# Kernel optimization log

Measured on AMD Instinct MI355X. Metric: run time of the kernel, lower is better.

## Reference

```python
import jax, jax.numpy as jnp
import numpy as np
import math


def _forward(x, f0, theta, sigma, theta0, fbs, mix, w1, b1, w2, b2, conv_w):
    B, I, H, W = x.shape          # config requires B == I == H (== W here)
    S, O, _ = f0.shape            # config requires O == 1
    # ---- log-Gabor filter bank, fully vectorized over (scale, out, in) ----
    yy = jnp.linspace(-1.0, 1.0, H)[:, None]   # meshgrid 'ij': y along rows
    xx = jnp.linspace(-1.0, 1.0, W)[None, :]
    r = jnp.sqrt(xx ** 2 + yy ** 2 + 1e-6)     # [H,W]
    phi = jnp.arctan2(yy, xx)                  # [H,W]
    lr = jnp.log(r)
    log_gabor = jnp.exp(-(lr - jnp.log(f0)[..., None, None]) ** 2
                        / (2.0 * jnp.log(sigma)[..., None, None] ** 2))
    angular = jnp.exp(-(phi - theta[..., None, None]) ** 2
                      / (2.0 * theta0[..., None, None] ** 2))
    filters = log_gabor * angular              # [S,O,I,H,W]
    # ---- FFT (torch fftshift default shifts ALL dims; jnp matches) ----
    xs = jnp.fft.fftshift(jnp.fft.fft2(x))     # [B,I,H,W] complex64
    # ---- frequency attention (two 1x1 convs + softmax over scales) ----
    h1 = jax.nn.relu(jnp.einsum('bchw,oc->bohw', jnp.abs(xs), w1)
                     + b1[None, :, None, None])
    aw = jax.nn.softmax(jnp.einsum('bchw,sc->bshw', h1, w2)
                        + b2[None, :, None, None], axis=1)   # [B,S,H,W]
    # ---- attention-weighted combine. Faithful to torch broadcasting with
    # O==1 and B==I: attended[0,b,i,h,w] = sum_s xs[b,i]*F[s,0,i]*aw[i,s] ----
    attended = jnp.einsum('bihw,sihw,ishw->bihw', xs, filters[:, 0], aw)[None]
    # ---- dynamic frequency band mask (torch slices dims 2,3 = (Cin,H)) ----
    s_idx = jnp.floor((fbs[0, :, 0] + 1.0) / 2.0 * H).astype(jnp.int32)  # [I]
    e_idx = jnp.floor((fbs[0, :, 1] + 1.0) / 2.0 * H).astype(jnp.int32)
    arI = jnp.arange(I)
    arH = jnp.arange(H)
    mk = (arI[None, :] >= s_idx[:, None]) & (arI[None, :] < e_idx[:, None])  # [J,I]
    mh = (arH[None, :] >= s_idx[:, None]) & (arH[None, :] < e_idx[:, None])  # [J,H]
    mask = (mk[:, :, None] & mh[:, None, :]).astype(x.dtype)                 # [J,I,H]
    attended = attended * mask[None, :, :, :, None]
    # ---- back to spatial domain ----
    x_filtered = jnp.fft.ifft2(jnp.fft.ifftshift(attended)).real  # [1,B,I,H,W]
    # ---- spatial 3x3 conv path ----
    x_spatial = jax.lax.conv_general_dilated(
        x, conv_w, window_strides=(1, 1), padding=((1, 1), (1, 1)),
        dimension_numbers=('NCHW', 'OIHW', 'NCHW'))               # [B,1,H,W]
    return mix * x_filtered + (1.0 - mix) * x_spatial[None]


def setup_inputs() -> dict:
    key = jax.random.key(0)
    ks = jax.random.split(key, 10)
    B = I = H = W = 64
    O, S, HID = 1, 3, 64
    PI = math.pi
    x = jax.random.normal(ks[0], (B, I, H, W), dtype=jnp.float32)
    f0 = jnp.ones((S, O, I), jnp.float32)
    theta0 = jnp.ones((S, O, I), jnp.float32)
    sigma = jax.random.uniform(ks[1], (S, O, I), jnp.float32) * PI
    theta = jax.random.uniform(ks[2], (S, O, I), jnp.float32) * PI
    fbs = jax.random.uniform(ks[3], (O, I, 2), jnp.float32)
    mix = jax.random.uniform(ks[4], (1,), jnp.float32)
    w1 = jax.random.normal(ks[5], (HID, I), jnp.float32) * 0.05
    b1 = jnp.zeros((HID,), jnp.float32)
    w2 = jax.random.normal(ks[6], (S, HID), jnp.float32) * 0.05
    b2 = jnp.zeros((S,), jnp.float32)
    conv_w = jax.random.normal(ks[7], (O, I, 3, 3), jnp.float32) / math.sqrt(I * 9)
    return {'x': x, 'f0': f0, 'theta': theta, 'sigma': sigma, 'theta0': theta0,
            'fbs': fbs, 'mix': mix, 'w1': w1, 'b1': b1, 'w2': w2, 'b2': b2,
            'conv_w': conv_w}


def reference(x, f0, theta, sigma, theta0, fbs, mix, w1, b1, w2, b2, conv_w):
    return _forward(x, f0, theta, sigma, theta0, fbs, mix, w1, b1, w2, b2, conv_w)
```

## Files before the change

### kernel.cpp

```cpp
#include <hip/hip_runtime.h>

#define PI_D 3.14159265358979323846

namespace {
constexpr float CT[33] = {
  1.0000000000f,  0.9951847267f,  0.9807852804f,  0.9569403357f,
  0.9238795325f,  0.8819212643f,  0.8314696123f,  0.7730104534f,
  0.7071067812f,  0.6343932842f,  0.5555702330f,  0.4713967368f,
  0.3826834324f,  0.2902846773f,  0.1950903220f,  0.0980171403f,
  0.0f,          -0.0980171403f, -0.1950903220f, -0.2902846773f,
 -0.3826834324f, -0.4713967368f, -0.5555702330f, -0.6343932842f,
 -0.7071067812f, -0.7730104534f, -0.8314696123f, -0.8819212643f,
 -0.9238795325f, -0.9569403357f, -0.9807852804f, -0.9951847267f,
 -1.0f};
constexpr float STb[33] = {
  0.0f,           0.0980171403f,  0.1950903220f,  0.2902846773f,
  0.3826834324f,  0.4713967368f,  0.5555702330f,  0.6343932842f,
  0.7071067812f,  0.7730104534f,  0.8314696123f,  0.8819212643f,
  0.9238795325f,  0.9569403357f,  0.9807852804f,  0.9951847267f,
  1.0f,           0.9951847267f,  0.9807852804f,  0.9569403357f,
  0.9238795325f,  0.8819212643f,  0.8314696123f,  0.7730104534f,
  0.7071067812f,  0.6343932842f,  0.5555702330f,  0.4713967368f,
  0.3826834324f,  0.2902846773f,  0.1950903220f,  0.0980171403f,
  0.0f};
}

__device__ __forceinline__ void bitrev64(float v[64]) {
#pragma unroll
  for (int i = 0; i < 64; ++i) {
    const int j = (int)(__brev((unsigned)i) >> 26);
    if (j > i) { const float tv = v[i]; v[i] = v[j]; v[j] = tv; }
  }
}

template <bool INV, bool REAL>
__device__ __forceinline__ void fft64_stages(float re[64], float im[64]) {
#pragma unroll
  for (int s = 0; s < 6; ++s) {
    const int half = 1 << s;
    const int m = half << 1;
    const int tstep = 32 >> s;
#pragma unroll
    for (int k = 0; k < 64; k += m) {
#pragma unroll
      for (int j = 0; j < half; ++j) {
        const int ti = j * tstep;
        const int a = k + j, b = k + j + half;
        if (REAL && j == 0) {
          const float tr = re[b];
          re[b] = re[a] - tr;
          re[a] = re[a] + tr;
        } else if (REAL && ti == 16) {
          const float t0 = re[b];
          re[b] = re[a];
          im[b] = t0;
          im[a] = -t0;
        } else {
          float tr, tii;
          if (ti == 0) {
            tr = re[b]; tii = im[b];
          } else if (ti == 16) {
            if (INV) { tr = -im[b]; tii = re[b]; }
            else     { tr =  im[b]; tii = -re[b]; }
          } else {
            const float wr = CT[ti];
            const float wi = INV ? STb[ti] : -STb[ti];
            tr  = re[b] * wr - im[b] * wi;
            tii = re[b] * wi + im[b] * wr;
          }
          re[b] = re[a] - tr;  im[b] = im[a] - tii;
          re[a] = re[a] + tr;  im[a] = im[a] + tii;
        }
      }
    }
  }
}

template <bool INV>
__device__ __forceinline__ void fft64_regs(float re[64], float im[64]) {
  bitrev64(re);
  bitrev64(im);
  fft64_stages<INV, false>(re, im);
}

__device__ __forceinline__ void fft64_fwd_real(float re[64], float im[64]) {
  bitrev64(re);
  fft64_stages<false, true>(re, im);
}

__device__ __forceinline__ void band_from_fbs(const float* __restrict__ fbs,
                                              int c, int& s0, int& e0) {
  s0 = (int)floorf((fbs[2 * c]     + 1.0f) * 0.5f * 64.0f);
  e0 = (int)floorf((fbs[2 * c + 1] + 1.0f) * 0.5f * 64.0f);
}

__global__ __launch_bounds__(64) void k_fft_fwd(const float* __restrict__ x,
                                                float* __restrict__ Mag,
                                                float* __restrict__ Fc,
                                                const float* __restrict__ fbs,
                                                const float* __restrict__ w1,
                                                float* __restrict__ w1T) {
  __shared__ float buf[64][65];
  const int t = threadIdx.x;
  const int img = blockIdx.x;
  if (img == 0) {
    for (int k = 0; k < 64; ++k) w1T[t * 64 + k] = w1[k * 64 + t];
  }
  const float* xp = x + ((size_t)img << 12);
  const float4* xr4 = reinterpret_cast<const float4*>(xp + (t << 6));
  float re[64], im[64];
#pragma unroll
  for (int q = 0; q < 16; ++q) {
    const float4 v = xr4[q];
    re[4 * q]     = v.x; re[4 * q + 1] = v.y;
    re[4 * q + 2] = v.z; re[4 * q + 3] = v.w;
  }
#pragma unroll
  for (int j = 0; j < 64; ++j) im[j] = 0.0f;
  fft64_fwd_real(re, im);
#pragma unroll
  for (int j = 0; j < 64; ++j) buf[t][j] = re[j];
  __syncthreads();
#pragma unroll
  for (int j = 0; j < 64; ++j) re[j] = buf[j][t];
  __syncthreads();
#pragma unroll
  for (int j = 0; j < 64; ++j) buf[t][j] = im[j];
  __syncthreads();
#pragma unroll
  for (int j = 0; j < 64; ++j) im[j] = buf[j][t];
  fft64_regs<false>(re, im);
  float* Mg = Mag + ((size_t)img << 12);
  Mg[t] = sqrtf(re[0] * re[0] + im[0] * im[0]);
#pragma unroll
  for (int j = 33; j < 64; ++j)
    Mg[j * 64 + t] = sqrtf(re[j] * re[j] + im[j] * im[j]);
  const int b = img >> 6, i = img & 63;
  const int b_s = (b + 32) & 63, i_s = (i + 32) & 63;
  int s0, e0;
  band_from_fbs(fbs, b_s, s0, e0);
  if ((i_s >= s0) && (i_s < e0)) {
    float* Fre = Fc + ((size_t)((b << 5) + i) << 13);
    float* Fim = Fre + 4096;
#pragma unroll
    for (int j = 0; j < 64; ++j) {
      Fre[j * 64 + t] = re[j];
      Fim[j * 64 + t] = im[j];
    }
  }
}

__global__ __launch_bounds__(256, 4) void k_attn_conv(
    const float* __restrict__ Mag, const float* __restrict__ w1T,
    const float* __restrict__ b1, const float* __restrict__ w2,
    const float* __restrict__ b2, const float* __restrict__ f0,
    const float* __restrict__ theta, const float* __restrict__ sigma,
    const float* __restrict__ theta0, const float* __restrict__ fbs,
    float* __restrict__ Wc,
    const float* __restrict__ x, const float* __restrict__ cw,
    const float* __restrict__ mixp, float* __restrict__ xsp,
    float* __restrict__ out) {
  __shared__ float part[4][3][64];
  const int t = threadIdx.x;
  const unsigned blk = blockIdx.x;
  const unsigned q3 = blk / 3u;
  const unsigned r3 = blk - q3 * 3u;

  if (r3 == 2u) {
    const int lane = t & 63;
    const int cwv = t >> 6;
    const int b = (int)(q3 >> 4);
    const int row = (int)((q3 & 15u) << 2) | cwv;
    const float* xb = x + ((size_t)b << 18);
    const int rm = row > 0 ? row - 1 : 0;
    const int rp = row < 63 ? row + 1 : 63;
    float P00 = 0.f, P01 = 0.f, P02 = 0.f;
    float P10 = 0.f, P11 = 0.f, P12 = 0.f;
    float P20 = 0.f, P21 = 0.f, P22 = 0.f;
#pragma unroll 4
    for (int ch = 0; ch < 64; ++ch) {
      const float* xc = xb + (ch << 12);
      const float v0 = xc[(rm << 6) + lane];
      const float v1 = xc[(row << 6) + lane];
      const float v2 = xc[(rp << 6) + lane];
      const float* wp = cw + ch * 9;
      P00 = fmaf(v0, wp[0], P00);
      P01 = fmaf(v0, wp[1], P01);
      P02 = fmaf(v0, wp[2], P02);
      P10 = fmaf(v1, wp[3], P10);
      P11 = fmaf(v1, wp[4], P11);
      P12 = fmaf(v1, wp[5], P12);
      P20 = fmaf(v2, wp[6], P20);
      P21 = fmaf(v2, wp[7], P21);
      P22 = fmaf(v2, wp[8], P22);
    }
    const float tmask = (row > 0) ? 1.0f : 0.0f;
    const float bmask = (row < 63) ? 1.0f : 0.0f;
    const float Ql = tmask * P00 + P10 + bmask * P20;
    const float Qm = tmask * P01 + P11 + bmask * P21;
    const float Qr = tmask * P02 + P12 + bmask * P22;
    const float fromL = __shfl_up(Ql, 1, 64);
    const float fromR = __shfl_down(Qr, 1, 64);
    float acc = Qm;
    if (lane > 0) acc += fromL;
    if (lane < 63) acc += fromR;
    xsp[((size_t)b << 12) + (row << 6) + lane] = acc;
    const int b_s = (b + 32) & 63;
    int s0, e0;
    band_from_fbs(fbs, b_s, s0, e0);
    const float val = (1.0f - mixp[0]) * acc;
    float* ob = out + ((size_t)b << 18) + (row << 6) + lane;
#pragma unroll 4
    for (int i2 = 0; i2 < 64; ++i2) {
      const int i_s = (i2 + 32) & 63;
      if (!(i_s >= s0 && i_s < e0)) ob[(size_t)i2 << 12] = val;
    }
    return;
  }

  const int ai = (int)(2u * q3 + r3);
  const int lane = t & 63;
  const int wv = __builtin_amdgcn_readfirstlane(t >> 6);
  const int k0 = wv << 4;
  const int i = ai >> 5;
  const int h = (ai & 31) + 1;
  const int b_f = (i + 32) & 63;
  const int u_f = (h + 32) & 63;
  const int v_f = (lane + 32) & 63;
  const int pos_f = (u_f << 6) + v_f;
  const float* Mb = Mag + (((size_t)(b_f << 6)) << 12) + pos_f;
  float acc[16];
#pragma unroll
  for (int k = 0; k < 16; ++k) acc[k] = 0.0f;
#pragma unroll 4
  for (int c = 0; c < 64; ++c) {
    const float mc = Mb[(size_t)((c + 32) & 63) << 12];
    const float* wrow = w1T + (c << 6) + k0;
#pragma unroll
    for (int k = 0; k < 16; ++k) acc[k] = fmaf(wrow[k], mc, acc[k]);
  }
  float p0 = 0.0f, p1 = 0.0f, p2 = 0.0f;
#pragma unroll
  for (int k = 0; k < 16; ++k) {
    const float hv = fmaxf(acc[k] + b1[k0 + k], 0.0f);
    p0 = fmaf(w2[k0 + k], hv, p0);
    p1 = fmaf(w2[64 + k0 + k], hv, p1);
    p2 = fmaf(w2[128 + k0 + k], hv, p2);
  }
  if (wv != 0) {
    part[wv][0][lane] = p0;
    part[wv][1][lane] = p1;
    part[wv][2][lane] = p2;
  }
  __syncthreads();
  if (wv != 0) return;
  float l0 = b2[0] + p0 + part[1][0][lane] + part[2][0][lane] + part[3][0][lane];
  float l1 = b2[1] + p1 + part[1][1][lane] + part[2][1][lane] + part[3][1][lane];
  float l2 = b2[2] + p2 + part[1][2][lane] + part[2][2][lane] + part[3][2][lane];
  float mx = fmaxf(l0, fmaxf(l1, l2));
  float e0v = expf(l0 - mx), e1 = expf(l1 - mx), e2 = expf(l2 - mx);
  float inv = 1.0f / (e0v + e1 + e2);
  float aw0 = e0v * inv, aw1 = e1 * inv, aw2 = e2 * inv;
  int hw = h;
  if (h != 32) {
    const int src = (64 - lane) & 63;
    aw0 = __shfl(aw0, src, 64);
    aw1 = __shfl(aw1, src, 64);
    aw2 = __shfl(aw2, src, 64);
    hw = 64 - h;
  }
  const float yy = -1.0f + (float)hw * (2.0f / 63.0f);
  const float xx = -1.0f + (float)lane * (2.0f / 63.0f);
  const float r = sqrtf(xx * xx + yy * yy + 1e-6f);
  const float lr = logf(r);
  const float phi = atan2f(yy, xx);
  float wc = 0.0f;
  const float aws[3] = {aw0, aw1, aw2};
#pragma unroll
  for (int s = 0; s < 3; ++s) {
    const float f0v = f0[s * 64 + i];
    const float sgv = sigma[s * 64 + i];
    const float thv = theta[s * 64 + i];
    const float t0v = theta0[s * 64 + i];
    const float ls = logf(sgv);
    const float d1 = lr - logf(f0v);
    const float g1 = expf(-(d1 * d1) / (2.0f * ls * ls));
    const float d2 = phi - thv;
    const float g2 = expf(-(d2 * d2) / (2.0f * t0v * t0v));
    wc = fmaf(g1 * g2, aws[s], wc);
  }
  Wc[((i << 6) + hw) * 64 + lane] = wc;
}

__global__ __launch_bounds__(64) void k_ifft_act(
    const float* __restrict__ Fc, const float* __restrict__ Wc,
    const float* __restrict__ xsp, const float* __restrict__ fbs,
    const float* __restrict__ mixp, float* __restrict__ out) {
  const int b = blockIdx.x >> 5;
  const int i = blockIdx.x & 31;
  const int b_s = (b + 32) & 63, i_s = i + 32;
  int s0, e0;
  band_from_fbs(fbs, b_s, s0, e0);
  if (!((i_s >= s0) && (i_s < e0))) return;
  __shared__ float buf[64][65];
  const int t = threadIdx.x;
  const float* Fre = Fc + ((size_t)((b << 5) + i) << 13);
  const float* Fim = Fre + 4096;
  const float* Wcp = Wc + ((size_t)i_s << 12);
  const int u_s = (t + 32) & 63;
  const bool act_row = (u_s >= s0 && u_s < e0);
  const float* wrow = Wcp + (u_s << 6);
  const float4* fr4 = reinterpret_cast<const float4*>(Fre + (t << 6));
  const float4* fi4 = reinterpret_cast<const float4*>(Fim + (t << 6));
  float re[64], im[64];
#pragma unroll
  for (int q = 0; q < 16; ++q) {
    const int j0 = 4 * q;
    const float4 w4 = act_row
        ? *reinterpret_cast<const float4*>(wrow + ((j0 + 32) & 63))
        : make_float4(0.0f, 0.0f, 0.0f, 0.0f);
    const float4 vr = fr4[q];
    const float4 vi = fi4[q];
    re[j0]     = vr.x * w4.x;  re[j0 + 1] = vr.y * w4.y;
    re[j0 + 2] = vr.z * w4.z;  re[j0 + 3] = vr.w * w4.w;
    im[j0]     = vi.x * w4.x;  im[j0 + 1] = vi.y * w4.y;
    im[j0 + 2] = vi.z * w4.z;  im[j0 + 3] = vi.w * w4.w;
  }
  fft64_regs<true>(re, im);
#pragma unroll
  for (int j = 0; j < 64; ++j) buf[t][j] = re[j];
  __syncthreads();
#pragma unroll
  for (int j = 0; j < 64; ++j) re[j] = buf[j][t];
  __syncthreads();
#pragma unroll
  for (int j = 0; j < 64; ++j) buf[t][j] = im[j];
  __syncthreads();
#pragma unroll
  for (int j = 0; j < 64; ++j) im[j] = buf[j][t];
  fft64_regs<true>(re, im);
  const float mixv = mixp[0];
  const float sc = mixv * (1.0f / 4096.0f);
  const float om = 1.0f - mixv;
  float* op = out + (((size_t)(b << 6) + i) << 12);
  const float* xp = xsp + ((size_t)b << 12);
#pragma unroll
  for (int j = 0; j < 64; ++j)
    op[j * 64 + t] = fmaf(sc, re[j], om * xp[j * 64 + t]);
}

extern "C" void kernel_launch(void* const* d_in, const int* in_sizes, int n_in,
                              void* d_out, int out_size, void* d_ws, size_t ws_size,
                              hipStream_t stream) {
  const float* x      = (const float*)d_in[0];
  const float* f0     = (const float*)d_in[1];
  const float* theta  = (const float*)d_in[2];
  const float* sigma  = (const float*)d_in[3];
  const float* theta0 = (const float*)d_in[4];
  const float* fbs    = (const float*)d_in[5];
  const float* mix    = (const float*)d_in[6];
  const float* w1     = (const float*)d_in[7];
  const float* b1     = (const float*)d_in[8];
  const float* w2     = (const float*)d_in[9];
  const float* b2     = (const float*)d_in[10];
  const float* cw     = (const float*)d_in[11];
  float* out = (float*)d_out;
  char* ws = (char*)d_ws;
  float* Mag = (float*)(ws);
  float* Fc  = (float*)(ws + 67108864);
  float* Wc  = (float*)(ws + 134217728);
  float* xsp = (float*)(ws + 134217728 + 1048576);
  float* w1T = (float*)(ws + 134217728 + 2097152);

  k_fft_fwd<<<4096, 64, 0, stream>>>(x, Mag, Fc, fbs, w1, w1T);
  k_attn_conv<<<3072, 256, 0, stream>>>(Mag, w1T, b1, w2, b2, f0, theta, sigma,
                                        theta0, fbs, Wc, x, cw, mix, xsp, out);
  k_ifft_act<<<2048, 64, 0, stream>>>(Fc, Wc, xsp, fbs, mix, out);
}
```

Measured before the change: 189.5 us.

## Move 3x3 conv into forward FFT kernel and remap attention blocks per XCD

```diff
diff --git a/kernel.cpp b/kernel.cpp
--- a/kernel.cpp
+++ b/kernel.cpp
@@ -94,15 +94,88 @@
   e0 = (int)floorf((fbs[2 * c + 1] + 1.0f) * 0.5f * 64.0f);
 }
 
-__global__ __launch_bounds__(64) void k_fft_fwd(const float* __restrict__ x,
-                                                float* __restrict__ Mag,
-                                                float* __restrict__ Fc,
-                                                const float* __restrict__ fbs,
-                                                const float* __restrict__ w1,
-                                                float* __restrict__ w1T) {
+__global__ __launch_bounds__(64) void k_fft_conv(
+    const float* __restrict__ x, float* __restrict__ Mag,
+    float* __restrict__ Fc, const float* __restrict__ fbs,
+    const float* __restrict__ w1, float* __restrict__ w1T,
+    const float* __restrict__ cw, const float* __restrict__ mixp,
+    float* __restrict__ xsp, float* __restrict__ out) {
   __shared__ float buf[64][65];
   const int t = threadIdx.x;
-  const int img = blockIdx.x;
+  const unsigned blk = blockIdx.x;
+  const unsigned q5 = blk / 5u;
+  const unsigned r5 = blk - q5 * 5u;
+
+  if (r5 == 4u) {
+    const int lane = t;
+    const int b = (int)(q5 >> 4);
+    const int r0 = (int)((q5 & 15u) << 2);
+    const float* xb = x + ((size_t)b << 18);
+    const int rm = r0 > 0 ? r0 - 1 : 0;
+    const int rp = r0 + 4 < 63 ? r0 + 4 : 63;
+    const float m0 = (r0 > 0) ? 1.0f : 0.0f;
+    const float m5 = (r0 + 4 <= 63) ? 1.0f : 0.0f;
+    float aL0 = 0.f, aM0 = 0.f, aR0 = 0.f;
+    float aL1 = 0.f, aM1 = 0.f, aR1 = 0.f;
+    float aL2 = 0.f, aM2 = 0.f, aR2 = 0.f;
+    float aL3 = 0.f, aM3 = 0.f, aR3 = 0.f;
+#pragma unroll 2
+    for (int ch = 0; ch < 64; ++ch) {
+      const float* xc = xb + (ch << 12);
+      const float v0 = m0 * xc[(rm << 6) + lane];
+      const float v1 = xc[((r0 + 0) << 6) + lane];
+      const float v2 = xc[((r0 + 1) << 6) + lane];
+      const float v3 = xc[((r0 + 2) << 6) + lane];
+      const float v4 = xc[((r0 + 3) << 6) + lane];
+      const float v5 = m5 * xc[(rp << 6) + lane];
+      const float* wp = cw + ch * 9;
+      aL0 = fmaf(v0, wp[0], fmaf(v1, wp[3], fmaf(v2, wp[6], aL0)));
+      aM0 = fmaf(v0, wp[1], fmaf(v1, wp[4], fmaf(v2, wp[7], aM0)));
+      aR0 = fmaf(v0, wp[2], fmaf(v1, wp[5], fmaf(v2, wp[8], aR0)));
+      aL1 = fmaf(v1, wp[0], fmaf(v2, wp[3], fmaf(v3, wp[6], aL1)));
+      aM1 = fmaf(v1, wp[1], fmaf(v2, wp[4], fmaf(v3, wp[7], aM1)));
+      aR1 = fmaf(v1, wp[2], fmaf(v2, wp[5], fmaf(v3, wp[8], aR1)));
+      aL2 = fmaf(v2, wp[0], fmaf(v3, wp[3], fmaf(v4, wp[6], aL2)));
+      aM2 = fmaf(v2, wp[1], fmaf(v3, wp[4], fmaf(v4, wp[7], aM2)));
+      aR2 = fmaf(v2, wp[2], fmaf(v3, wp[5], fmaf(v4, wp[8], aR2)));
+      aL3 = fmaf(v3, wp[0], fmaf(v4, wp[3], fmaf(v5, wp[6], aL3)));
+      aM3 = fmaf(v3, wp[1], fmaf(v4, wp[4], fmaf(v5, wp[7], aM3)));
+      aR3 = fmaf(v3, wp[2], fmaf(v4, wp[5], fmaf(v5, wp[8], aR3)));
+    }
+    const int b_s = (b + 32) & 63;
+    int s0, e0;
+    band_from_fbs(fbs, b_s, s0, e0);
+    const float omix = 1.0f - mixp[0];
+    float accQ[4];
+    {
+      const float QL[4] = {aL0, aL1, aL2, aL3};
+      const float QM[4] = {aM0, aM1, aM2, aM3};
+      const float QR[4] = {aR0, aR1, aR2, aR3};
+#pragma unroll
+      for (int q = 0; q < 4; ++q) {
+        const float fromL = __shfl_up(QL[q], 1, 64);
+        const float fromR = __shfl_down(QR[q], 1, 64);
+        float acc = QM[q];
+        if (lane > 0) acc += fromL;
+        if (lane < 63) acc += fromR;
+        accQ[q] = acc;
+        xsp[((size_t)b << 12) + ((r0 + q) << 6) + lane] = acc;
+      }
+    }
+#pragma unroll
+    for (int q = 0; q < 4; ++q) {
+      const float val = omix * accQ[q];
+      float* ob = out + ((size_t)b << 18) + ((r0 + q) << 6) + lane;
+#pragma unroll 4
+      for (int i2 = 0; i2 < 64; ++i2) {
+        const int i_s = (i2 + 32) & 63;
+        if (!(i_s >= s0 && i_s < e0)) ob[(size_t)i2 << 12] = val;
+      }
+    }
+    return;
+  }
+
+  const int img = (int)(4u * q5 + r5);
   if (img == 0) {
     for (int k = 0; k < 64; ++k) w1T[t * 64 + k] = w1[k * 64 + t];
   }
@@ -150,75 +223,18 @@
   }
 }
 
-__global__ __launch_bounds__(256, 4) void k_attn_conv(
+__global__ __launch_bounds__(256, 8) void k_attn(
     const float* __restrict__ Mag, const float* __restrict__ w1T,
     const float* __restrict__ b1, const float* __restrict__ w2,
     const float* __restrict__ b2, const float* __restrict__ f0,
     const float* __restrict__ theta, const float* __restrict__ sigma,
     const float* __restrict__ theta0, const float* __restrict__ fbs,
-    float* __restrict__ Wc,
-    const float* __restrict__ x, const float* __restrict__ cw,
-    const float* __restrict__ mixp, float* __restrict__ xsp,
-    float* __restrict__ out) {
+    float* __restrict__ Wc) {
   __shared__ float part[4][3][64];
   const int t = threadIdx.x;
-  const unsigned blk = blockIdx.x;
-  const unsigned q3 = blk / 3u;
-  const unsigned r3 = blk - q3 * 3u;
-
-  if (r3 == 2u) {
-    const int lane = t & 63;
-    const int cwv = t >> 6;
-    const int b = (int)(q3 >> 4);
-    const int row = (int)((q3 & 15u) << 2) | cwv;
-    const float* xb = x + ((size_t)b << 18);
-    const int rm = row > 0 ? row - 1 : 0;
-    const int rp = row < 63 ? row + 1 : 63;
-    float P00 = 0.f, P01 = 0.f, P02 = 0.f;
-    float P10 = 0.f, P11 = 0.f, P12 = 0.f;
-    float P20 = 0.f, P21 = 0.f, P22 = 0.f;
-#pragma unroll 4
-    for (int ch = 0; ch < 64; ++ch) {
-      const float* xc = xb + (ch << 12);
-      const float v0 = xc[(rm << 6) + lane];
-      const float v1 = xc[(row << 6) + lane];
-      const float v2 = xc[(rp << 6) + lane];
-      const float* wp = cw + ch * 9;
-      P00 = fmaf(v0, wp[0], P00);
-      P01 = fmaf(v0, wp[1], P01);
-      P02 = fmaf(v0, wp[2], P02);
-      P10 = fmaf(v1, wp[3], P10);
-      P11 = fmaf(v1, wp[4], P11);
-      P12 = fmaf(v1, wp[5], P12);
-      P20 = fmaf(v2, wp[6], P20);
-      P21 = fmaf(v2, wp[7], P21);
-      P22 = fmaf(v2, wp[8], P22);
-    }
-    const float tmask = (row > 0) ? 1.0f : 0.0f;
-    const float bmask = (row < 63) ? 1.0f : 0.0f;
-    const float Ql = tmask * P00 + P10 + bmask * P20;
-    const float Qm = tmask * P01 + P11 + bmask * P21;
-    const float Qr = tmask * P02 + P12 + bmask * P22;
-    const float fromL = __shfl_up(Ql, 1, 64);
-    const float fromR = __shfl_down(Qr, 1, 64);
-    float acc = Qm;
-    if (lane > 0) acc += fromL;
-    if (lane < 63) acc += fromR;
-    xsp[((size_t)b << 12) + (row << 6) + lane] = acc;
-    const int b_s = (b + 32) & 63;
-    int s0, e0;
-    band_from_fbs(fbs, b_s, s0, e0);
-    const float val = (1.0f - mixp[0]) * acc;
-    float* ob = out + ((size_t)b << 18) + (row << 6) + lane;
-#pragma unroll 4
-    for (int i2 = 0; i2 < 64; ++i2) {
-      const int i_s = (i2 + 32) & 63;
-      if (!(i_s >= s0 && i_s < e0)) ob[(size_t)i2 << 12] = val;
-    }
-    return;
-  }
-
-  const int ai = (int)(2u * q3 + r3);
+  const unsigned bid = blockIdx.x;
+  const unsigned m = bid >> 3, xcd = bid & 7u;
+  const int ai = (int)(((((m >> 5) << 3) + xcd) << 5) | (m & 31u));
   const int lane = t & 63;
   const int wv = __builtin_amdgcn_readfirstlane(t >> 6);
   const int k0 = wv << 4;
@@ -372,8 +388,9 @@
   float* xsp = (float*)(ws + 134217728 + 1048576);
   float* w1T = (float*)(ws + 134217728 + 2097152);
 
-  k_fft_fwd<<<4096, 64, 0, stream>>>(x, Mag, Fc, fbs, w1, w1T);
-  k_attn_conv<<<3072, 256, 0, stream>>>(Mag, w1T, b1, w2, b2, f0, theta, sigma,
-                                        theta0, fbs, Wc, x, cw, mix, xsp, out);
+  k_fft_conv<<<5120, 64, 0, stream>>>(x, Mag, Fc, fbs, w1, w1T, cw, mix,
+                                      xsp, out);
+  k_attn<<<2048, 256, 0, stream>>>(Mag, w1T, b1, w2, b2, f0, theta, sigma,
+                                   theta0, fbs, Wc);
   k_ifft_act<<<2048, 64, 0, stream>>>(Fc, Wc, xsp, fbs, mix, out);
 }
```

After: 201.7 us. 6.5% more time.
